# Optimization experiments

Hardware: AMD Instinct MI355X
Metric: run time of the kernel (lower is better)

Reference implementation:

```python
import jax, jax.numpy as jnp
import numpy as np

N = 50000   # nodes
E = 800000  # edges (avg degree 16)
DIMS = [(128, 128), (128, 128), (128, 64)]  # (in, out) per SAGEConv layer
EPS_BN = 1e-5
EPS_NORM = 1e-12


def _make_layer(key, din, dout):
    k1, k2 = jax.random.split(key)
    s = 1.0 / np.sqrt(din)
    return (
        jax.random.normal(k1, (dout, din), jnp.float32) * s,  # Wl: neighbor linear
        jnp.zeros((dout,), jnp.float32),                      # bl
        jax.random.normal(k2, (dout, din), jnp.float32) * s,  # Wr: root linear (no bias in PyG)
        jnp.ones((dout,), jnp.float32),                       # bn gamma
        jnp.zeros((dout,), jnp.float32),                      # bn beta
        jnp.zeros((dout,), jnp.float32),                      # bn running mean
        jnp.ones((dout,), jnp.float32),                       # bn running var
    )


def setup_inputs() -> dict:
    key = jax.random.key(0)
    kx, ke, k0, k1, k2 = jax.random.split(key, 5)
    inp = {
        "x": jax.random.normal(kx, (N, 128), jnp.float32),
        "edge_index": jax.random.randint(ke, (2, E), 0, N, dtype=jnp.int32),
    }
    for i, (k, (din, dout)) in enumerate(zip([k0, k1, k2], DIMS)):
        Wl, bl, Wr, g, b, rm, rv = _make_layer(k, din, dout)
        inp.update({f"Wl{i}": Wl, f"bl{i}": bl, f"Wr{i}": Wr,
                    f"g{i}": g, f"b{i}": b, f"rm{i}": rm, f"rv{i}": rv})
    return inp


def _sage_conv(x, src, dst, Wl, bl, Wr):
    # mean aggregation of incoming messages: gather src features, scatter-add at dst
    agg = jax.ops.segment_sum(x[src], dst, num_segments=N)          # [N, din]
    deg = jax.ops.segment_sum(jnp.ones((src.shape[0],), x.dtype), dst, num_segments=N)
    mean = agg / jnp.maximum(deg, 1.0)[:, None]
    return mean @ Wl.T + bl + x @ Wr.T


def _bn_eval(x, g, b, rm, rv):
    return g * (x - rm) * jax.lax.rsqrt(rv + EPS_BN) + b


def reference(x, edge_index,
              Wl0, bl0, Wr0, g0, b0, rm0, rv0,
              Wl1, bl1, Wr1, g1, b1, rm1, rv1,
              Wl2, bl2, Wr2, g2, b2, rm2, rv2):
    src, dst = edge_index[0], edge_index[1]
    layers = [
        (Wl0, bl0, Wr0, g0, b0, rm0, rv0),
        (Wl1, bl1, Wr1, g1, b1, rm1, rv1),
        (Wl2, bl2, Wr2, g2, b2, rm2, rv2),
    ]
    h = x
    for i, (Wl, bl, Wr, g, b, rm, rv) in enumerate(layers):
        h = _bn_eval(_sage_conv(h, src, dst, Wl, bl, Wr), g, b, rm, rv)
        if i < len(layers) - 1:
            h = jax.nn.relu(h)  # dropout is identity in eval mode
    # F.normalize(p=2, dim=1)
    return h / jnp.maximum(jnp.linalg.norm(h, axis=1, keepdims=True), EPS_NORM)
```

## Files before the change

### kernel.cpp

```cpp
#include <hip/hip_runtime.h>
#include <hip/hip_bf16.h>

#define CDIV(a,b) (((a)+(b)-1)/(b))
#define NBUCK_MAX 512
#define BUCK_CAP 3072
#define FUSE_CAP 1536
#define CAPL     4096
#define AGGF_CAP 2048

typedef __attribute__((ext_vector_type(8))) short short8;
typedef __attribute__((ext_vector_type(4))) float f32x4;
typedef __attribute__((ext_vector_type(2))) float f32x2;

static __device__ __forceinline__ unsigned short f2bf(float f){
  union { float f; unsigned u; } v; v.f = f;
  unsigned r = v.u + 0x7fffu + ((v.u >> 16) & 1u);
  return (unsigned short)(r >> 16);
}
static __device__ __forceinline__ unsigned pack2(float lo, float hi){
  return (unsigned)f2bf(lo) | ((unsigned)f2bf(hi) << 16);
}
static __device__ __forceinline__ float bf2f(unsigned short s){
  union { unsigned u; float f; } v; v.u = ((unsigned)s) << 16; return v.f;
}
static __device__ __forceinline__ unsigned pk_fp8x4(float a, float b, float c, float d){
  int v = __builtin_amdgcn_cvt_pk_fp8_f32(a, b, 0, false);
  v = __builtin_amdgcn_cvt_pk_fp8_f32(c, d, v, true);
  return (unsigned)v;
}

#define ACCP16(v) { b0 += __builtin_amdgcn_cvt_pk_f32_fp8((int)v.x, false); \
                    b1 += __builtin_amdgcn_cvt_pk_f32_fp8((int)v.x, true);  \
                    b2 += __builtin_amdgcn_cvt_pk_f32_fp8((int)v.y, false); \
                    b3 += __builtin_amdgcn_cvt_pk_f32_fp8((int)v.y, true);  \
                    b4 += __builtin_amdgcn_cvt_pk_f32_fp8((int)v.z, false); \
                    b5 += __builtin_amdgcn_cvt_pk_f32_fp8((int)v.z, true);  \
                    b6 += __builtin_amdgcn_cvt_pk_f32_fp8((int)v.w, false); \
                    b7 += __builtin_amdgcn_cvt_pk_f32_fp8((int)v.w, true); }


struct WtpArgs {
  const float *W0, *W1, *bl, *g, *b, *rm, *rv;
  unsigned short* Bpk; float *sc; float *sh;
  int kblk, dout, do_bn, nblk, perm;
};

static __device__ __forceinline__ void wtp_one(const WtpArgs& a, int idx){
  int NB16 = a.kblk*32*a.dout;
  if (idx < NB16){
    int j = idx & 7, lane = (idx >> 3) & 63, rest = idx >> 9;
    int NT = a.dout >> 4;
    int nt = rest % NT, kk = rest / NT;
    int nn = nt*16 + (lane & 15);
    int k  = kk*32 + ((lane >> 4) * 8) + j;
    float v;
    if (k < 128){
      int kc = a.perm ? (((k & 7) << 4) | (k >> 3)) : k;
      v = a.W0[nn*128 + kc];
    } else {
      v = a.W1[nn*128 + (k - 128)];
    }
    a.Bpk[idx] = f2bf(v);
  } else if (a.do_bn && idx < NB16 + a.dout){
    int jj = idx - NB16;
    float s = a.g[jj] * rsqrtf(a.rv[jj] + 1e-5f);
    a.sc[jj] = s;
    a.sh[jj] = (a.bl[jj] - a.rm[jj]) * s + a.b[jj];
  }
}


__global__ __launch_bounds__(256) void k_prep(const float* __restrict__ x, int n4, unsigned* __restrict__ xb,
                                              unsigned* __restrict__ xq,
                                              const int* __restrict__ esrc, const int* __restrict__ edst,
                                              int E, int* __restrict__ bcur, int* __restrict__ ovCnt,
                                              unsigned* __restrict__ ebuf, unsigned* __restrict__ ovBuf,
                                              int nbuck, int castBlocks, int binBlocks,
                                              WtpArgs a0, WtpArgs a1, WtpArgs a2, WtpArgs a3){
  __shared__ int scnt[NBUCK_MAX];
  __shared__ int sbase[NBUCK_MAX];
  int b = blockIdx.x, t = threadIdx.x;
  if (b < castBlocks){
    int i0 = b*1024 + t;
    #pragma unroll
    for (int j=0;j<4;j++){
      int i = i0 + j*256;
      if (i < n4){
        float4 v = ((const float4*)x)[i];
        uint2 o; o.x = pack2(v.x, v.y); o.y = pack2(v.z, v.w);
        ((uint2*)xb)[i] = o;
        xq[i] = pk_fp8x4(v.x, v.y, v.z, v.w);
      }
    }
    return;
  }
  b -= castBlocks;
  if (b < binBlocks){
    for (int i=t;i<nbuck;i+=256) scnt[i] = 0;
    __syncthreads();
    constexpr int EPT = 16;
    int e0 = b*256*EPT;
    int bb[EPT]; unsigned pk[EPT];
    #pragma unroll
    for (int i=0;i<EPT;i++){
      int e = e0 + i*256 + t;
      if (e < E){
        int d = edst[e];
        bb[i] = d >> 7;
        pk[i] = ((unsigned)(d & 127) << 16) | (unsigned)esrc[e];
        atomicAdd(&scnt[bb[i]], 1);
      } else bb[i] = -1;
    }
    __syncthreads();
    for (int i=t;i<nbuck;i+=256){
      int c = scnt[i];
      sbase[i] = (c > 0) ? atomicAdd(&bcur[i], c) : 0;
      scnt[i] = 0;
    }
    __syncthreads();
    #pragma unroll
    for (int i=0;i<EPT;i++){
      if (bb[i] >= 0){
        int p = atomicAdd(&scnt[bb[i]], 1);
        int gpos = sbase[bb[i]] + p;
        if (gpos < BUCK_CAP) ebuf[(size_t)bb[i]*BUCK_CAP + gpos] = pk[i];
        else { int oi = atomicAdd(ovCnt, 1); ovBuf[oi] = ((unsigned)bb[i] << 23) | pk[i]; }
      }
    }
    return;
  }
  b -= binBlocks;
  if (b < a0.nblk){ wtp_one(a0, b*256 + t); return; }
  b -= a0.nblk;
  if (b < a1.nblk){ wtp_one(a1, b*256 + t); return; }
  b -= a1.nblk;
  if (b < a2.nblk){ wtp_one(a2, b*256 + t); return; }
  b -= a2.nblk;
  wtp_one(a3, b*256 + t);
}


__global__ __launch_bounds__(256, 4) void k_bfuse(
    const unsigned* __restrict__ ebuf, const int* __restrict__ bcur,
    const int* __restrict__ ovCnt, const unsigned* __restrict__ ovBuf, int N,
    int* __restrict__ off, int* __restrict__ deg, int* __restrict__ csr,
    const uint4* __restrict__ xq4, const unsigned short* __restrict__ Ag,
    const unsigned short* __restrict__ Bpk, const float* __restrict__ sc, const float* __restrict__ sh,
    unsigned short* __restrict__ outh, unsigned* __restrict__ outq){
  __shared__ uint4 Ms4[64*17];
  __shared__ int scsr[FUSE_CAP];
  unsigned short* Ms = (unsigned short*)Ms4;
  int* sdeg = (int*)Ms4;
  int* sabs = sdeg + 128;
  int* cur  = sabs + 129;
  int wb = blockIdx.x;
  int b = wb >> 1, hi = wb & 1;
  int t = threadIdx.x;
  if (t < 128){ sdeg[t] = 0; cur[t] = 0; }
  __syncthreads();
  size_t bBase = (size_t)b*BUCK_CAP;
  int cntMain = min(bcur[b], BUCK_CAP);
  int ov = *ovCnt;
  for (int e = t; e < cntMain; e += 256)
    atomicAdd(&sdeg[ebuf[bBase + e] >> 16], 1);
  for (int i = t; i < ov; i += 256){
    unsigned v = ovBuf[i];
    if ((int)(v >> 23) == b) atomicAdd(&sdeg[(v >> 16) & 127u], 1);
  }
  __syncthreads();
  for (int d=1; d<128; d<<=1){
    int u = (t < 128 && t >= d) ? sdeg[t-d] : 0;
    __syncthreads();
    if (t < 128) sdeg[t] += u;
    __syncthreads();
  }
  if (t == 0) sabs[0] = 0;
  if (t < 128) sabs[t+1] = sdeg[t];
  __syncthreads();
  int base64 = sabs[hi*64];
  int myTot  = sabs[hi*64 + 64] - base64;
  int n0 = (b << 7) + hi*64;
  int cnt = (N > n0) ? min(64, N - n0) : 0;
  if (t < cnt){
    off[n0 + t] = (int)bBase + sabs[hi*64 + t];
    deg[n0 + t] = sabs[hi*64 + t + 1] - sabs[hi*64 + t];
  }
  int lane = t & 63, w = t >> 6, sl = lane & 7;
  int gs0[2], gs1[2];
  #pragma unroll
  for (int it=0; it<2; it++){
    int rk = w*16 + it*8 + (lane >> 3);
    gs0[it] = sabs[hi*64 + rk] - base64;
    gs1[it] = sabs[hi*64 + rk + 1] - base64;
  }
  bool fits = myTot <= FUSE_CAP;
  for (int e = t; e < cntMain; e += 256){
    unsigned pr = ebuf[bBase + e];
    int ln = (int)(pr >> 16);
    if ((ln >> 6) == hi){
      int p = atomicAdd(&cur[ln], 1);
      int gpos = sabs[ln] + p;
      int sv = (int)(pr & 0xffffu);
      if (fits) scsr[gpos - base64] = sv;
      else      csr[bBase + gpos] = sv;
    }
  }
  for (int i = t; i < ov; i += 256){
    unsigned v = ovBuf[i];
    if ((int)(v >> 23) == b){
      int ln = (int)((v >> 16) & 127u);
      if ((ln >> 6) == hi){
        int p = atomicAdd(&cur[ln], 1);
        int gpos = sabs[ln] + p;
        int sv = (int)(v & 0xffffu);
        if (fits) scsr[gpos - base64] = sv;
        else      csr[bBase + gpos] = sv;
      }
    }
  }
  __syncthreads();
  const int* gcsr = csr + bBase + base64;
  if (fits){
    for (int i = t; i < myTot; i += 256) csr[bBase + base64 + i] = scsr[i];
  } else {
    for (int i = t; i < FUSE_CAP; i += 256) scsr[i] = gcsr[i];
    __syncthreads();
  }

  #pragma unroll
  for (int it=0; it<2; it++){
    int rk = w*16 + it*8 + (lane >> 3);
    int s0 = gs0[it], s1 = gs1[it];
    f32x2 b0={0,0},b1={0,0},b2={0,0},b3={0,0},b4={0,0},b5={0,0},b6={0,0},b7={0,0};
    int e = s0;
    for (; e + 8 <= s1; e += 8){
      int i0,i1,i2,i3,i4,i5,i6,i7;
      if (e + 8 <= FUSE_CAP){
        i0 = scsr[e];   i1 = scsr[e+1]; i2 = scsr[e+2]; i3 = scsr[e+3];
        i4 = scsr[e+4]; i5 = scsr[e+5]; i6 = scsr[e+6]; i7 = scsr[e+7];
      } else {
        i0 = gcsr[e];   i1 = gcsr[e+1]; i2 = gcsr[e+2]; i3 = gcsr[e+3];
        i4 = gcsr[e+4]; i5 = gcsr[e+5]; i6 = gcsr[e+6]; i7 = gcsr[e+7];
      }
      uint4 v0 = xq4[(size_t)i0*8 + sl];
      uint4 v1 = xq4[(size_t)i1*8 + sl];
      uint4 v2 = xq4[(size_t)i2*8 + sl];
      uint4 v3 = xq4[(size_t)i3*8 + sl];
      uint4 v4 = xq4[(size_t)i4*8 + sl];
      uint4 v5 = xq4[(size_t)i5*8 + sl];
      uint4 v6 = xq4[(size_t)i6*8 + sl];
      uint4 v7 = xq4[(size_t)i7*8 + sl];
      ACCP16(v0); ACCP16(v1); ACCP16(v2); ACCP16(v3);
      ACCP16(v4); ACCP16(v5); ACCP16(v6); ACCP16(v7);
    }
    for (; e + 4 <= s1; e += 4){
      int i0,i1,i2,i3;
      if (e + 4 <= FUSE_CAP){
        i0 = scsr[e]; i1 = scsr[e+1]; i2 = scsr[e+2]; i3 = scsr[e+3];
      } else {
        i0 = gcsr[e]; i1 = gcsr[e+1]; i2 = gcsr[e+2]; i3 = gcsr[e+3];
      }
      uint4 v0 = xq4[(size_t)i0*8 + sl];
      uint4 v1 = xq4[(size_t)i1*8 + sl];
      uint4 v2 = xq4[(size_t)i2*8 + sl];
      uint4 v3 = xq4[(size_t)i3*8 + sl];
      ACCP16(v0); ACCP16(v1); ACCP16(v2); ACCP16(v3);
    }
    for (; e < s1; e++){
      int ii = (e < FUSE_CAP) ? scsr[e] : gcsr[e];
      uint4 v = xq4[(size_t)ii*8 + sl];
      ACCP16(v);
    }
    int d = s1 - s0;
    float inv = 1.0f / (float)(d > 0 ? d : 1);
    uint4 o0, o1;
    o0.x = pack2(b0.x*inv, b0.y*inv);  o0.y = pack2(b1.x*inv, b1.y*inv);
    o0.z = pack2(b2.x*inv, b2.y*inv);  o0.w = pack2(b3.x*inv, b3.y*inv);
    o1.x = pack2(b4.x*inv, b4.y*inv);  o1.y = pack2(b5.x*inv, b5.y*inv);
    o1.z = pack2(b6.x*inv, b6.y*inv);  o1.w = pack2(b7.x*inv, b7.y*inv);
    Ms4[rk*17 + sl*2]     = o0;
    Ms4[rk*17 + sl*2 + 1] = o1;
  }
  __syncthreads();

  int quad = lane >> 4, c = lane & 15;
  int woff = w*16;
  int r0 = n0 + woff + c;

  f32x4 acc[8];
  #pragma unroll
  for (int nt=0;nt<8;nt++) acc[nt] = (f32x4){0.f,0.f,0.f,0.f};

  #pragma unroll
  for (int kk=0; kk<8; kk++){
    int ka = (kk & 3)*32 + quad*8;
    short8 a0;
    if (kk < 4){
      a0 = *(const short8*)&Ms[(woff + c)*136 + ka];
    } else {
      a0 = (short8){0,0,0,0,0,0,0,0};
      if (r0 < N) a0 = *(const short8*)(Ag + (size_t)r0*128 + ka);
    }
    #pragma unroll
    for (int nt=0; nt<8; nt++){
      short8 bb2 = *(const short8*)(Bpk + (size_t)((kk*8 + nt)*64 + lane)*8);
      acc[nt] = __builtin_amdgcn_mfma_f32_16x16x32_bf16(a0, bb2, acc[nt], 0, 0, 0);
    }
  }

  float scv[8], shv[8];
  #pragma unroll
  for (int nt=0;nt<8;nt++){ scv[nt] = sc[nt*16 + c]; shv[nt] = sh[nt*16 + c]; }

  #pragma unroll
  for (int r=0;r<4;r++){
    int row = n0 + woff + quad*4 + r;
    if (row < N){
      float u[8];
      #pragma unroll
      for (int nt=0;nt<8;nt++){
        float uu = acc[nt][r]*scv[nt] + shv[nt];
        u[nt] = fmaxf(uu, 0.f);
        outh[(size_t)row*128 + nt*16 + c] = f2bf(u[nt]);
      }
      uint2 q;
      q.x = pk_fp8x4(u[0], u[1], u[2], u[3]);
      q.y = pk_fp8x4(u[4], u[5], u[6], u[7]);
      ((uint2*)outq)[(size_t)row*16 + c] = q;
    }
  }
}


__global__ __launch_bounds__(256, 4) void k_fuse1(
    const uint4* __restrict__ hq4, const int* __restrict__ off, const int* __restrict__ deg,
    const int* __restrict__ csr,
    const unsigned short* __restrict__ Ag, const unsigned short* __restrict__ Bpk,
    const float* __restrict__ sc, const float* __restrict__ sh,
    const unsigned short* __restrict__ BpkL,
    unsigned short* __restrict__ outh, unsigned* __restrict__ outyl, int n){
  __shared__ uint4 Ms4[64*17];
  __shared__ uint4 sBL4[1024];
  __shared__ int sw[2];
  unsigned short* Ms = (unsigned short*)Ms4;
  int* scsr = (int*)sBL4;
  int t = threadIdx.x;
  int n0 = blockIdx.x*64;
  if (t == 0){
    sw[0] = off[n0];
    int last = min(n0 + 63, n - 1);
    sw[1] = off[last] + deg[last];
  }
  __syncthreads();
  int e0b = sw[0];
  int span = sw[1] - e0b;
  for (int i = t; i < span && i < CAPL; i += 256) scsr[i] = csr[e0b + i];
  __syncthreads();

  int lane = t & 63, w = t >> 6;
  int sl = lane & 7;

  #pragma unroll
  for (int it=0; it<2; it++){
    int rk = w*16 + it*8 + (lane >> 3);
    int idx = n0 + rk;
    bool valid = idx < n;
    int s0 = valid ? off[idx] : 0;
    int s1 = valid ? (s0 + deg[idx]) : 0;
    f32x2 b0={0,0},b1={0,0},b2={0,0},b3={0,0},b4={0,0},b5={0,0},b6={0,0},b7={0,0};
    int e = s0;
    for (; e + 8 <= s1; e += 8){
      int le = e - e0b;
      int i0,i1,i2,i3,i4,i5,i6,i7;
      if (le + 8 <= CAPL){
        i0 = scsr[le];   i1 = scsr[le+1]; i2 = scsr[le+2]; i3 = scsr[le+3];
        i4 = scsr[le+4]; i5 = scsr[le+5]; i6 = scsr[le+6]; i7 = scsr[le+7];
      } else {
        i0 = csr[e];   i1 = csr[e+1]; i2 = csr[e+2]; i3 = csr[e+3];
        i4 = csr[e+4]; i5 = csr[e+5]; i6 = csr[e+6]; i7 = csr[e+7];
      }
      uint4 v0 = hq4[(size_t)i0*8 + sl];
      uint4 v1 = hq4[(size_t)i1*8 + sl];
      uint4 v2 = hq4[(size_t)i2*8 + sl];
      uint4 v3 = hq4[(size_t)i3*8 + sl];
      uint4 v4 = hq4[(size_t)i4*8 + sl];
      uint4 v5 = hq4[(size_t)i5*8 + sl];
      uint4 v6 = hq4[(size_t)i6*8 + sl];
      uint4 v7 = hq4[(size_t)i7*8 + sl];
      ACCP16(v0); ACCP16(v1); ACCP16(v2); ACCP16(v3);
      ACCP16(v4); ACCP16(v5); ACCP16(v6); ACCP16(v7);
    }
    for (; e + 4 <= s1; e += 4){
      int le = e - e0b;
      int i0,i1,i2,i3;
      if (le + 4 <= CAPL){
        i0 = scsr[le]; i1 = scsr[le+1]; i2 = scsr[le+2]; i3 = scsr[le+3];
      } else {
        i0 = csr[e]; i1 = csr[e+1]; i2 = csr[e+2]; i3 = csr[e+3];
      }
      uint4 v0 = hq4[(size_t)i0*8 + sl];
      uint4 v1 = hq4[(size_t)i1*8 + sl];
      uint4 v2 = hq4[(size_t)i2*8 + sl];
      uint4 v3 = hq4[(size_t)i3*8 + sl];
      ACCP16(v0); ACCP16(v1); ACCP16(v2); ACCP16(v3);
    }
    for (; e < s1; e++){
      int le = e - e0b;
      int ii = (le < CAPL) ? scsr[le] : csr[e];
      uint4 v = hq4[(size_t)ii*8 + sl];
      ACCP16(v);
    }
    int d = s1 - s0;
    float inv = 1.0f / (float)(d > 0 ? d : 1);
    uint4 o0, o1;
    o0.x = pack2(b0.x*inv, b0.y*inv);  o0.y = pack2(b1.x*inv, b1.y*inv);
    o0.z = pack2(b2.x*inv, b2.y*inv);  o0.w = pack2(b3.x*inv, b3.y*inv);
    o1.x = pack2(b4.x*inv, b4.y*inv);  o1.y = pack2(b5.x*inv, b5.y*inv);
    o1.z = pack2(b6.x*inv, b6.y*inv);  o1.w = pack2(b7.x*inv, b7.y*inv);
    Ms4[rk*17 + sl*2]     = o0;
    Ms4[rk*17 + sl*2 + 1] = o1;
  }
  __syncthreads();

  int quad = lane >> 4, c = lane & 15;
  int woff = w*16;
  int r0 = n0 + woff + c;

  f32x4 acc[8];
  #pragma unroll
  for (int nt=0;nt<8;nt++) acc[nt] = (f32x4){0.f,0.f,0.f,0.f};

  #pragma unroll
  for (int kk=0; kk<8; kk++){
    int ka = (kk & 3)*32 + quad*8;
    short8 a0;
    if (kk < 4){
      a0 = *(const short8*)&Ms[(woff + c)*136 + ka];
    } else {
      a0 = (short8){0,0,0,0,0,0,0,0};
      if (r0 < n) a0 = *(const short8*)(Ag + (size_t)r0*128 + ka);
    }
    #pragma unroll
    for (int nt=0; nt<8; nt++){
      short8 bb2 = *(const short8*)(Bpk + (size_t)((kk*8 + nt)*64 + lane)*8);
      acc[nt] = __builtin_amdgcn_mfma_f32_16x16x32_bf16(a0, bb2, acc[nt], 0, 0, 0);
    }
  }

  float scv[8], shv[8];
  #pragma unroll
  for (int nt=0;nt<8;nt++){ scv[nt] = sc[nt*16 + c]; shv[nt] = sh[nt*16 + c]; }

  __syncthreads();

  #pragma unroll
  for (int r=0;r<4;r++){
    int lrow = woff + quad*4 + r;
    int row = n0 + lrow;
    if (row < n){
      float u[8];
      #pragma unroll
      for (int nt=0;nt<8;nt++){
        float uu = acc[nt][r]*scv[nt] + shv[nt];
        u[nt] = fmaxf(uu, 0.f);
        outh[(size_t)row*128 + nt*16 + c] = f2bf(u[nt]);
      }
      #pragma unroll
      for (int nt=0;nt<8;nt++) Ms[lrow*136 + nt*16 + c] = f2bf(u[nt]);
    } else {
      #pragma unroll
      for (int nt=0;nt<8;nt++) Ms[lrow*136 + nt*16 + c] = 0;
    }
  }

  {
    const uint4* sL = (const uint4*)BpkL;
    #pragma unroll
    for (int i=0;i<4;i++) sBL4[i*256 + t] = sL[i*256 + t];
  }
  __syncthreads();
  unsigned short* BsL = (unsigned short*)sBL4;
  f32x4 acc2[4];
  #pragma unroll
  for (int nt=0;nt<4;nt++) acc2[nt] = (f32x4){0.f,0.f,0.f,0.f};
  int r0l = woff + c;
  #pragma unroll
  for (int kk=0; kk<4; kk++){
    int ka = kk*32 + quad*8;
    short8 a0 = *(const short8*)&Ms[r0l*136 + ka];
    #pragma unroll
    for (int nt=0; nt<4; nt++){
      short8 bb2 = *(const short8*)&BsL[(size_t)((kk*4 + nt)*64 + lane)*8];
      acc2[nt] = __builtin_amdgcn_mfma_f32_16x16x32_bf16(a0, bb2, acc2[nt], 0, 0, 0);
    }
  }
  #pragma unroll
  for (int r=0;r<4;r++){
    int row = n0 + woff + quad*4 + r;
    if (row < n){
      unsigned q = pk_fp8x4(acc2[0][r], acc2[1][r], acc2[2][r], acc2[3][r]);
      outyl[(size_t)row*16 + c] = q;
    }
  }
}


__global__ __launch_bounds__(256, 4) void k_aggf(
    const uint4* __restrict__ ylq4, const int* __restrict__ off, const int* __restrict__ deg,
    const int* __restrict__ csr,
    const unsigned short* __restrict__ A0, const unsigned short* __restrict__ BpkR,
    const float* __restrict__ sc, const float* __restrict__ sh,
    float* __restrict__ outf, int n){
  __shared__ unsigned short Ms[64*64];
  __shared__ unsigned short Bs[128*64];
  __shared__ int scsr[AGGF_CAP];
  __shared__ int sw[2];
  int t = threadIdx.x;
  int n0 = blockIdx.x*64;
  if (t == 0){
    sw[0] = off[n0];
    int last = min(n0 + 63, n - 1);
    sw[1] = off[last] + deg[last];
  }
  {
    const uint4* s = (const uint4*)BpkR;
    uint4* d = (uint4*)Bs;
    #pragma unroll
    for (int i=0;i<4;i++) d[i*256 + t] = s[i*256 + t];
  }
  __syncthreads();
  int e0b = sw[0];
  int span = sw[1] - e0b;
  for (int i = t; i < span && i < AGGF_CAP; i += 256) scsr[i] = csr[e0b + i];
  __syncthreads();

  int lane = t & 63, w = t >> 6;
  int sl4 = lane & 3;

  {
    int rk = w*16 + (lane >> 2);
    int idx = n0 + rk;
    bool valid = idx < n;
    int s0 = valid ? off[idx] : 0;
    int s1 = valid ? (s0 + deg[idx]) : 0;
    f32x2 b0={0,0},b1={0,0},b2={0,0},b3={0,0},b4={0,0},b5={0,0},b6={0,0},b7={0,0};
    int e = s0;
    for (; e + 8 <= s1; e += 8){
      int le = e - e0b;
      int i0,i1,i2,i3,i4,i5,i6,i7;
      if (le + 8 <= AGGF_CAP){
        i0 = scsr[le];   i1 = scsr[le+1]; i2 = scsr[le+2]; i3 = scsr[le+3];
        i4 = scsr[le+4]; i5 = scsr[le+5]; i6 = scsr[le+6]; i7 = scsr[le+7];
      } else {
        i0 = csr[e];   i1 = csr[e+1]; i2 = csr[e+2]; i3 = csr[e+3];
        i4 = csr[e+4]; i5 = csr[e+5]; i6 = csr[e+6]; i7 = csr[e+7];
      }
      uint4 v0 = ylq4[(size_t)i0*4 + sl4];
      uint4 v1 = ylq4[(size_t)i1*4 + sl4];
      uint4 v2 = ylq4[(size_t)i2*4 + sl4];
      uint4 v3 = ylq4[(size_t)i3*4 + sl4];
      uint4 v4 = ylq4[(size_t)i4*4 + sl4];
      uint4 v5 = ylq4[(size_t)i5*4 + sl4];
      uint4 v6 = ylq4[(size_t)i6*4 + sl4];
      uint4 v7 = ylq4[(size_t)i7*4 + sl4];
      ACCP16(v0); ACCP16(v1); ACCP16(v2); ACCP16(v3);
      ACCP16(v4); ACCP16(v5); ACCP16(v6); ACCP16(v7);
    }
    for (; e + 4 <= s1; e += 4){
      int le = e - e0b;
      int i0,i1,i2,i3;
      if (le + 4 <= AGGF_CAP){
        i0 = scsr[le]; i1 = scsr[le+1]; i2 = scsr[le+2]; i3 = scsr[le+3];
      } else {
        i0 = csr[e]; i1 = csr[e+1]; i2 = csr[e+2]; i3 = csr[e+3];
      }
      uint4 v0 = ylq4[(size_t)i0*4 + sl4];
      uint4 v1 = ylq4[(size_t)i1*4 + sl4];
      uint4 v2 = ylq4[(size_t)i2*4 + sl4];
      uint4 v3 = ylq4[(size_t)i3*4 + sl4];
      ACCP16(v0); ACCP16(v1); ACCP16(v2); ACCP16(v3);
    }
    for (; e < s1; e++){
      int le = e - e0b;
      int ii = (le < AGGF_CAP) ? scsr[le] : csr[e];
      uint4 v = ylq4[(size_t)ii*4 + sl4];
      ACCP16(v);
    }
    int d = s1 - s0;
    float inv = 1.0f / (float)(d > 0 ? d : 1);
    uint4 o0, o1;
    o0.x = pack2(b0.x*inv, b0.y*inv);  o0.y = pack2(b1.x*inv, b1.y*inv);
    o0.z = pack2(b2.x*inv, b2.y*inv);  o0.w = pack2(b3.x*inv, b3.y*inv);
    o1.x = pack2(b4.x*inv, b4.y*inv);  o1.y = pack2(b5.x*inv, b5.y*inv);
    o1.z = pack2(b6.x*inv, b6.y*inv);  o1.w = pack2(b7.x*inv, b7.y*inv);
    ((uint4*)Ms)[rk*8 + sl4*2]     = o0;
    ((uint4*)Ms)[rk*8 + sl4*2 + 1] = o1;
  }
  __syncthreads();

  int quad = lane >> 4, c = lane & 15;
  int woff = w*16;
  int r0 = n0 + woff + c;
  f32x4 acc[4];
  #pragma unroll
  for (int nt=0;nt<4;nt++) acc[nt] = (f32x4){0.f,0.f,0.f,0.f};
  #pragma unroll
  for (int kk=0; kk<4; kk++){
    int ka = kk*32 + quad*8;
    short8 a0 = {0,0,0,0,0,0,0,0};
    if (r0 < n) a0 = *(const short8*)(A0 + (size_t)r0*128 + ka);
    #pragma unroll
    for (int nt=0; nt<4; nt++){
      short8 bb2 = *(const short8*)&Bs[(size_t)((kk*4 + nt)*64 + lane)*8];
      acc[nt] = __builtin_amdgcn_mfma_f32_16x16x32_bf16(a0, bb2, acc[nt], 0, 0, 0);
    }
  }

  float scv[4], shv[4];
  #pragma unroll
  for (int nt=0;nt<4;nt++){ scv[nt] = sc[nt*16 + c]; shv[nt] = sh[nt*16 + c]; }

  #pragma unroll
  for (int r=0;r<4;r++){
    int lr = woff + quad*4 + r;
    int row = n0 + lr;
    float v[4];
    float ss2 = 0.f;
    if (row < n){
      #pragma unroll
      for (int nt=0;nt<4;nt++){
        float u = acc[nt][r] + bf2f(Ms[lr*64 + c*4 + nt]);
        u = u*scv[nt] + shv[nt];
        v[nt] = u;
        ss2 += u*u;
      }
    } else {
      #pragma unroll
      for (int nt=0;nt<4;nt++) v[nt] = 0.f;
    }
    ss2 += __shfl_xor(ss2, 1, 64);
    ss2 += __shfl_xor(ss2, 2, 64);
    ss2 += __shfl_xor(ss2, 4, 64);
    ss2 += __shfl_xor(ss2, 8, 64);
    float rn = 1.0f / fmaxf(sqrtf(ss2), 1e-12f);
    if (row < n){
      #pragma unroll
      for (int nt=0;nt<4;nt++) outf[(size_t)row*64 + nt*16 + c] = v[nt]*rn;
    }
  }
}


extern "C" void kernel_launch(void* const* d_in, const int* in_sizes, int n_in,
                              void* d_out, int out_size, void* d_ws, size_t ws_size,
                              hipStream_t stream){
  const float* x = (const float*)d_in[0];
  const int* ei  = (const int*)d_in[1];
  int N = in_sizes[0] / 128;
  int E = in_sizes[1] / 2;
  const int* esrc = ei;
  const int* edst = ei + E;
  int nbuck = CDIV(N, 128);
  int nb2 = 2*nbuck;

  const float *Wl[3], *bl[3], *Wr[3], *g[3], *bb[3], *rm[3], *rv[3];
  int dout[3];
  for (int i=0;i<3;i++){
    int base = 2 + 7*i;
    Wl[i]=(const float*)d_in[base];   bl[i]=(const float*)d_in[base+1];
    Wr[i]=(const float*)d_in[base+2]; g[i] =(const float*)d_in[base+3];
    bb[i]=(const float*)d_in[base+4]; rm[i]=(const float*)d_in[base+5];
    rv[i]=(const float*)d_in[base+6];
    dout[i] = in_sizes[base] / 128;
  }

  char* p = (char*)d_ws;
  size_t o = 0;
  auto alloc = [&](size_t bytes)->void*{ void* r = p + o; o += (bytes + 255) & ~(size_t)255; return r; };
  int* bz    = (int*)alloc((size_t)(nbuck + 1)*4);
  int* bcur  = bz;
  int* ovCnt = bz + nbuck;
  int* off   = (int*)alloc((size_t)N*4);
  int* deg   = (int*)alloc((size_t)N*4);
  int* csr   = (int*)alloc((size_t)nbuck*BUCK_CAP*4);
  unsigned* ebuf  = (unsigned*)alloc((size_t)nbuck*BUCK_CAP*4);
  unsigned* ovBuf = (unsigned*)alloc((size_t)E*4);
  unsigned* xb   = (unsigned*)alloc((size_t)N*64*4);
  unsigned* xq   = (unsigned*)alloc((size_t)N*128);
  unsigned* h_a  = (unsigned*)alloc((size_t)N*64*4);
  unsigned* haq  = (unsigned*)alloc((size_t)N*128);
  unsigned* h_b  = (unsigned*)alloc((size_t)N*64*4);
  unsigned* ylb  = (unsigned*)alloc((size_t)N*64);
  unsigned short* Bpk01[2];
  float* sc[3]; float* sh[3];
  for (int i=0;i<2;i++) Bpk01[i] = (unsigned short*)alloc((size_t)256*dout[i]*2);
  unsigned short* BpkL = (unsigned short*)alloc((size_t)128*dout[2]*2);
  unsigned short* BpkR = (unsigned short*)alloc((size_t)128*dout[2]*2);
  for (int i=0;i<3;i++){
    sc[i] = (float*)alloc((size_t)dout[i]*4);
    sh[i] = (float*)alloc((size_t)dout[i]*4);
  }

  hipMemsetAsync(bz, 0, (size_t)(nbuck + 1)*4, stream);

  WtpArgs wa[4];
  wa[0] = { Wl[0], Wr[0], bl[0], g[0], bb[0], rm[0], rv[0], Bpk01[0], sc[0], sh[0], 8, dout[0], 1, CDIV(256*dout[0]+dout[0],256), 0 };
  wa[1] = { Wl[1], Wr[1], bl[1], g[1], bb[1], rm[1], rv[1], Bpk01[1], sc[1], sh[1], 8, dout[1], 1, CDIV(256*dout[1]+dout[1],256), 1 };
  wa[2] = { Wl[2], nullptr, nullptr, nullptr, nullptr, nullptr, nullptr, BpkL, nullptr, nullptr, 4, dout[2], 0, CDIV(128*dout[2],256), 0 };
  wa[3] = { Wr[2], nullptr, bl[2], g[2], bb[2], rm[2], rv[2], BpkR, sc[2], sh[2], 4, dout[2], 1, CDIV(128*dout[2]+dout[2],256), 0 };

  int castBlocks = CDIV(N*32, 256*4);
  int binBlocks  = CDIV(E, 256*16);
  int prepBlocks = castBlocks + binBlocks + wa[0].nblk + wa[1].nblk + wa[2].nblk + wa[3].nblk;
  k_prep<<<prepBlocks,256,0,stream>>>(x, N*32, xb, xq, esrc, edst, E, bcur, ovCnt, ebuf, ovBuf,
                                      nbuck, castBlocks, binBlocks,
                                      wa[0], wa[1], wa[2], wa[3]);

  k_bfuse<<<nb2,256,0,stream>>>(ebuf, bcur, ovCnt, ovBuf, N, off, deg, csr,
                                (const uint4*)xq, (const unsigned short*)xb,
                                Bpk01[0], sc[0], sh[0],
                                (unsigned short*)h_a, haq);
  k_fuse1<<<nb2,256,0,stream>>>((const uint4*)haq, off, deg, csr,
                                (const unsigned short*)h_a, Bpk01[1], sc[1], sh[1], BpkL,
                                (unsigned short*)h_b, ylb, N);
  k_aggf<<<nb2,256,0,stream>>>((const uint4*)ylb, off, deg, csr,
                               (const unsigned short*)h_b, BpkR, sc[2], sh[2],
                               (float*)d_out, N);
}
```

Measured before the change: 209.6 us.

## Replace bucketed CSR build with fixed-capacity per-node 16-bit adjacency slots

```diff
diff --git a/kernel.cpp b/kernel.cpp
--- a/kernel.cpp
+++ b/kernel.cpp
@@ -2,11 +2,7 @@
 #include <hip/hip_bf16.h>
 
 #define CDIV(a,b) (((a)+(b)-1)/(b))
-#define NBUCK_MAX 512
-#define BUCK_CAP 3072
-#define FUSE_CAP 1536
-#define CAPL     4096
-#define AGGF_CAP 2048
+#define NODE_CAP 64
 
 typedef __attribute__((ext_vector_type(8))) short short8;
 typedef __attribute__((ext_vector_type(4))) float f32x4;
@@ -37,6 +33,11 @@
                     b5 += __builtin_amdgcn_cvt_pk_f32_fp8((int)v.z, true);  \
                     b6 += __builtin_amdgcn_cvt_pk_f32_fp8((int)v.w, false); \
                     b7 += __builtin_amdgcn_cvt_pk_f32_fp8((int)v.w, true); }
+
+#define IDX8(iv) int i0 = (int)(iv.x & 0xffffu), i1 = (int)(iv.x >> 16), \
+                     i2 = (int)(iv.y & 0xffffu), i3 = (int)(iv.y >> 16), \
+                     i4 = (int)(iv.z & 0xffffu), i5 = (int)(iv.z >> 16), \
+                     i6 = (int)(iv.w & 0xffffu), i7 = (int)(iv.w >> 16)
 
 
 struct WtpArgs {
@@ -73,12 +74,10 @@
 __global__ __launch_bounds__(256) void k_prep(const float* __restrict__ x, int n4, unsigned* __restrict__ xb,
                                               unsigned* __restrict__ xq,
                                               const int* __restrict__ esrc, const int* __restrict__ edst,
-                                              int E, int* __restrict__ bcur, int* __restrict__ ovCnt,
-                                              unsigned* __restrict__ ebuf, unsigned* __restrict__ ovBuf,
-                                              int nbuck, int castBlocks, int binBlocks,
+                                              int E, int* __restrict__ deg, int* __restrict__ ovCnt,
+                                              unsigned short* __restrict__ csr16, unsigned* __restrict__ ovBuf,
+                                              int castBlocks, int binBlocks,
                                               WtpArgs a0, WtpArgs a1, WtpArgs a2, WtpArgs a3){
-  __shared__ int scnt[NBUCK_MAX];
-  __shared__ int sbase[NBUCK_MAX];
   int b = blockIdx.x, t = threadIdx.x;
   if (b < castBlocks){
     int i0 = b*1024 + t;
@@ -96,35 +95,17 @@
   }
   b -= castBlocks;
   if (b < binBlocks){
-    for (int i=t;i<nbuck;i+=256) scnt[i] = 0;
-    __syncthreads();
     constexpr int EPT = 16;
     int e0 = b*256*EPT;
-    int bb[EPT]; unsigned pk[EPT];
     #pragma unroll
     for (int i=0;i<EPT;i++){
       int e = e0 + i*256 + t;
       if (e < E){
         int d = edst[e];
-        bb[i] = d >> 7;
-        pk[i] = ((unsigned)(d & 127) << 16) | (unsigned)esrc[e];
-        atomicAdd(&scnt[bb[i]], 1);
-      } else bb[i] = -1;
-    }
-    __syncthreads();
-    for (int i=t;i<nbuck;i+=256){
-      int c = scnt[i];
-      sbase[i] = (c > 0) ? atomicAdd(&bcur[i], c) : 0;
-      scnt[i] = 0;
-    }
-    __syncthreads();
-    #pragma unroll
-    for (int i=0;i<EPT;i++){
-      if (bb[i] >= 0){
-        int p = atomicAdd(&scnt[bb[i]], 1);
-        int gpos = sbase[bb[i]] + p;
-        if (gpos < BUCK_CAP) ebuf[(size_t)bb[i]*BUCK_CAP + gpos] = pk[i];
-        else { int oi = atomicAdd(ovCnt, 1); ovBuf[oi] = ((unsigned)bb[i] << 23) | pk[i]; }
+        int s = esrc[e];
+        int p = atomicAdd(&deg[d], 1);
+        if (p < NODE_CAP) csr16[(size_t)d*NODE_CAP + p] = (unsigned short)s;
+        else { int oi = atomicAdd(ovCnt, 1); ovBuf[oi] = ((unsigned)d << 16) | (unsigned)s; }
       }
     }
     return;
@@ -140,108 +121,39 @@
 }
 
 
-__global__ __launch_bounds__(256, 4) void k_bfuse(
-    const unsigned* __restrict__ ebuf, const int* __restrict__ bcur,
+__global__ __launch_bounds__(256, 4) void k_fuse0(
+    const unsigned short* __restrict__ csr16, const int* __restrict__ deg,
     const int* __restrict__ ovCnt, const unsigned* __restrict__ ovBuf, int N,
-    int* __restrict__ off, int* __restrict__ deg, int* __restrict__ csr,
     const uint4* __restrict__ xq4, const unsigned short* __restrict__ Ag,
     const unsigned short* __restrict__ Bpk, const float* __restrict__ sc, const float* __restrict__ sh,
     unsigned short* __restrict__ outh, unsigned* __restrict__ outq){
   __shared__ uint4 Ms4[64*17];
-  __shared__ int scsr[FUSE_CAP];
+  __shared__ uint4 sc4[512];
   unsigned short* Ms = (unsigned short*)Ms4;
-  int* sdeg = (int*)Ms4;
-  int* sabs = sdeg + 128;
-  int* cur  = sabs + 129;
-  int wb = blockIdx.x;
-  int b = wb >> 1, hi = wb & 1;
+  unsigned short* scsr = (unsigned short*)sc4;
   int t = threadIdx.x;
-  if (t < 128){ sdeg[t] = 0; cur[t] = 0; }
-  __syncthreads();
-  size_t bBase = (size_t)b*BUCK_CAP;
-  int cntMain = min(bcur[b], BUCK_CAP);
+  int n0 = blockIdx.x*64;
+  {
+    const uint4* s = (const uint4*)(csr16 + (size_t)n0*NODE_CAP);
+    sc4[t] = s[t];
+    sc4[256 + t] = s[256 + t];
+  }
+  __syncthreads();
+
+  int lane = t & 63, w = t >> 6, sl = lane & 7;
   int ov = *ovCnt;
-  for (int e = t; e < cntMain; e += 256)
-    atomicAdd(&sdeg[ebuf[bBase + e] >> 16], 1);
-  for (int i = t; i < ov; i += 256){
-    unsigned v = ovBuf[i];
-    if ((int)(v >> 23) == b) atomicAdd(&sdeg[(v >> 16) & 127u], 1);
-  }
-  __syncthreads();
-  for (int d=1; d<128; d<<=1){
-    int u = (t < 128 && t >= d) ? sdeg[t-d] : 0;
-    __syncthreads();
-    if (t < 128) sdeg[t] += u;
-    __syncthreads();
-  }
-  if (t == 0) sabs[0] = 0;
-  if (t < 128) sabs[t+1] = sdeg[t];
-  __syncthreads();
-  int base64 = sabs[hi*64];
-  int myTot  = sabs[hi*64 + 64] - base64;
-  int n0 = (b << 7) + hi*64;
-  int cnt = (N > n0) ? min(64, N - n0) : 0;
-  if (t < cnt){
-    off[n0 + t] = (int)bBase + sabs[hi*64 + t];
-    deg[n0 + t] = sabs[hi*64 + t + 1] - sabs[hi*64 + t];
-  }
-  int lane = t & 63, w = t >> 6, sl = lane & 7;
-  int gs0[2], gs1[2];
+
   #pragma unroll
   for (int it=0; it<2; it++){
     int rk = w*16 + it*8 + (lane >> 3);
-    gs0[it] = sabs[hi*64 + rk] - base64;
-    gs1[it] = sabs[hi*64 + rk + 1] - base64;
-  }
-  bool fits = myTot <= FUSE_CAP;
-  for (int e = t; e < cntMain; e += 256){
-    unsigned pr = ebuf[bBase + e];
-    int ln = (int)(pr >> 16);
-    if ((ln >> 6) == hi){
-      int p = atomicAdd(&cur[ln], 1);
-      int gpos = sabs[ln] + p;
-      int sv = (int)(pr & 0xffffu);
-      if (fits) scsr[gpos - base64] = sv;
-      else      csr[bBase + gpos] = sv;
-    }
-  }
-  for (int i = t; i < ov; i += 256){
-    unsigned v = ovBuf[i];
-    if ((int)(v >> 23) == b){
-      int ln = (int)((v >> 16) & 127u);
-      if ((ln >> 6) == hi){
-        int p = atomicAdd(&cur[ln], 1);
-        int gpos = sabs[ln] + p;
-        int sv = (int)(v & 0xffffu);
-        if (fits) scsr[gpos - base64] = sv;
-        else      csr[bBase + gpos] = sv;
-      }
-    }
-  }
-  __syncthreads();
-  const int* gcsr = csr + bBase + base64;
-  if (fits){
-    for (int i = t; i < myTot; i += 256) csr[bBase + base64 + i] = scsr[i];
-  } else {
-    for (int i = t; i < FUSE_CAP; i += 256) scsr[i] = gcsr[i];
-    __syncthreads();
-  }
-
-  #pragma unroll
-  for (int it=0; it<2; it++){
-    int rk = w*16 + it*8 + (lane >> 3);
-    int s0 = gs0[it], s1 = gs1[it];
+    int node = n0 + rk;
+    int d = (node < N) ? deg[node] : 0;
+    int dmin = min(d, NODE_CAP);
     f32x2 b0={0,0},b1={0,0},b2={0,0},b3={0,0},b4={0,0},b5={0,0},b6={0,0},b7={0,0};
-    int e = s0;
-    for (; e + 8 <= s1; e += 8){
-      int i0,i1,i2,i3,i4,i5,i6,i7;
-      if (e + 8 <= FUSE_CAP){
-        i0 = scsr[e];   i1 = scsr[e+1]; i2 = scsr[e+2]; i3 = scsr[e+3];
-        i4 = scsr[e+4]; i5 = scsr[e+5]; i6 = scsr[e+6]; i7 = scsr[e+7];
-      } else {
-        i0 = gcsr[e];   i1 = gcsr[e+1]; i2 = gcsr[e+2]; i3 = gcsr[e+3];
-        i4 = gcsr[e+4]; i5 = gcsr[e+5]; i6 = gcsr[e+6]; i7 = gcsr[e+7];
-      }
+    int e = 0;
+    for (; e + 8 <= dmin; e += 8){
+      uint4 iv = *(const uint4*)&scsr[rk*NODE_CAP + e];
+      IDX8(iv);
       uint4 v0 = xq4[(size_t)i0*8 + sl];
       uint4 v1 = xq4[(size_t)i1*8 + sl];
       uint4 v2 = xq4[(size_t)i2*8 + sl];
@@ -253,25 +165,20 @@
       ACCP16(v0); ACCP16(v1); ACCP16(v2); ACCP16(v3);
       ACCP16(v4); ACCP16(v5); ACCP16(v6); ACCP16(v7);
     }
-    for (; e + 4 <= s1; e += 4){
-      int i0,i1,i2,i3;
-      if (e + 4 <= FUSE_CAP){
-        i0 = scsr[e]; i1 = scsr[e+1]; i2 = scsr[e+2]; i3 = scsr[e+3];
-      } else {
-        i0 = gcsr[e]; i1 = gcsr[e+1]; i2 = gcsr[e+2]; i3 = gcsr[e+3];
-      }
-      uint4 v0 = xq4[(size_t)i0*8 + sl];
-      uint4 v1 = xq4[(size_t)i1*8 + sl];
-      uint4 v2 = xq4[(size_t)i2*8 + sl];
-      uint4 v3 = xq4[(size_t)i3*8 + sl];
-      ACCP16(v0); ACCP16(v1); ACCP16(v2); ACCP16(v3);
-    }
-    for (; e < s1; e++){
-      int ii = (e < FUSE_CAP) ? scsr[e] : gcsr[e];
+    for (; e < dmin; e++){
+      int ii = (int)scsr[rk*NODE_CAP + e];
       uint4 v = xq4[(size_t)ii*8 + sl];
       ACCP16(v);
     }
-    int d = s1 - s0;
+    if (ov > 0 && d > NODE_CAP){
+      for (int i=0;i<ov;i++){
+        unsigned vv = ovBuf[i];
+        if ((int)(vv >> 16) == node){
+          uint4 v = xq4[(size_t)(vv & 0xffffu)*8 + sl];
+          ACCP16(v);
+        }
+      }
+    }
     float inv = 1.0f / (float)(d > 0 ? d : 1);
     uint4 o0, o1;
     o0.x = pack2(b0.x*inv, b0.y*inv);  o0.y = pack2(b1.x*inv, b1.y*inv);
@@ -333,52 +240,39 @@
 
 
 __global__ __launch_bounds__(256, 4) void k_fuse1(
-    const uint4* __restrict__ hq4, const int* __restrict__ off, const int* __restrict__ deg,
-    const int* __restrict__ csr,
+    const uint4* __restrict__ hq4, const unsigned short* __restrict__ csr16, const int* __restrict__ deg,
+    const int* __restrict__ ovCnt, const unsigned* __restrict__ ovBuf,
     const unsigned short* __restrict__ Ag, const unsigned short* __restrict__ Bpk,
     const float* __restrict__ sc, const float* __restrict__ sh,
     const unsigned short* __restrict__ BpkL,
     unsigned short* __restrict__ outh, unsigned* __restrict__ outyl, int n){
   __shared__ uint4 Ms4[64*17];
   __shared__ uint4 sBL4[1024];
-  __shared__ int sw[2];
   unsigned short* Ms = (unsigned short*)Ms4;
-  int* scsr = (int*)sBL4;
+  unsigned short* scsr = (unsigned short*)sBL4;
   int t = threadIdx.x;
   int n0 = blockIdx.x*64;
-  if (t == 0){
-    sw[0] = off[n0];
-    int last = min(n0 + 63, n - 1);
-    sw[1] = off[last] + deg[last];
-  }
-  __syncthreads();
-  int e0b = sw[0];
-  int span = sw[1] - e0b;
-  for (int i = t; i < span && i < CAPL; i += 256) scsr[i] = csr[e0b + i];
-  __syncthreads();
-
-  int lane = t & 63, w = t >> 6;
-  int sl = lane & 7;
+  {
+    const uint4* s = (const uint4*)(csr16 + (size_t)n0*NODE_CAP);
+    sBL4[t] = s[t];
+    sBL4[256 + t] = s[256 + t];
+  }
+  __syncthreads();
+
+  int lane = t & 63, w = t >> 6, sl = lane & 7;
+  int ov = *ovCnt;
 
   #pragma unroll
   for (int it=0; it<2; it++){
     int rk = w*16 + it*8 + (lane >> 3);
-    int idx = n0 + rk;
-    bool valid = idx < n;
-    int s0 = valid ? off[idx] : 0;
-    int s1 = valid ? (s0 + deg[idx]) : 0;
+    int node = n0 + rk;
+    int d = (node < n) ? deg[node] : 0;
+    int dmin = min(d, NODE_CAP);
     f32x2 b0={0,0},b1={0,0},b2={0,0},b3={0,0},b4={0,0},b5={0,0},b6={0,0},b7={0,0};
-    int e = s0;
-    for (; e + 8 <= s1; e += 8){
-      int le = e - e0b;
-      int i0,i1,i2,i3,i4,i5,i6,i7;
-      if (le + 8 <= CAPL){
-        i0 = scsr[le];   i1 = scsr[le+1]; i2 = scsr[le+2]; i3 = scsr[le+3];
-        i4 = scsr[le+4]; i5 = scsr[le+5]; i6 = scsr[le+6]; i7 = scsr[le+7];
-      } else {
-        i0 = csr[e];   i1 = csr[e+1]; i2 = csr[e+2]; i3 = csr[e+3];
-        i4 = csr[e+4]; i5 = csr[e+5]; i6 = csr[e+6]; i7 = csr[e+7];
-      }
+    int e = 0;
+    for (; e + 8 <= dmin; e += 8){
+      uint4 iv = *(const uint4*)&scsr[rk*NODE_CAP + e];
+      IDX8(iv);
       uint4 v0 = hq4[(size_t)i0*8 + sl];
       uint4 v1 = hq4[(size_t)i1*8 + sl];
       uint4 v2 = hq4[(size_t)i2*8 + sl];
@@ -390,27 +284,20 @@
       ACCP16(v0); ACCP16(v1); ACCP16(v2); ACCP16(v3);
       ACCP16(v4); ACCP16(v5); ACCP16(v6); ACCP16(v7);
     }
-    for (; e + 4 <= s1; e += 4){
-      int le = e - e0b;
-      int i0,i1,i2,i3;
-      if (le + 4 <= CAPL){
-        i0 = scsr[le]; i1 = scsr[le+1]; i2 = scsr[le+2]; i3 = scsr[le+3];
-      } else {
-        i0 = csr[e]; i1 = csr[e+1]; i2 = csr[e+2]; i3 = csr[e+3];
-      }
-      uint4 v0 = hq4[(size_t)i0*8 + sl];
-      uint4 v1 = hq4[(size_t)i1*8 + sl];
-      uint4 v2 = hq4[(size_t)i2*8 + sl];
-      uint4 v3 = hq4[(size_t)i3*8 + sl];
-      ACCP16(v0); ACCP16(v1); ACCP16(v2); ACCP16(v3);
-    }
-    for (; e < s1; e++){
-      int le = e - e0b;
-      int ii = (le < CAPL) ? scsr[le] : csr[e];
+    for (; e < dmin; e++){
+      int ii = (int)scsr[rk*NODE_CAP + e];
       uint4 v = hq4[(size_t)ii*8 + sl];
       ACCP16(v);
     }
-    int d = s1 - s0;
+    if (ov > 0 && d > NODE_CAP){
+      for (int i=0;i<ov;i++){
+        unsigned vv = ovBuf[i];
+        if ((int)(vv >> 16) == node){
+          uint4 v = hq4[(size_t)(vv & 0xffffu)*8 + sl];
+          ACCP16(v);
+        }
+      }
+    }
     float inv = 1.0f / (float)(d > 0 ? d : 1);
     uint4 o0, o1;
     o0.x = pack2(b0.x*inv, b0.y*inv);  o0.y = pack2(b1.x*inv, b1.y*inv);
@@ -506,55 +393,44 @@
 
 
 __global__ __launch_bounds__(256, 4) void k_aggf(
-    const uint4* __restrict__ ylq4, const int* __restrict__ off, const int* __restrict__ deg,
-    const int* __restrict__ csr,
+    const uint4* __restrict__ ylq4, const unsigned short* __restrict__ csr16, const int* __restrict__ deg,
+    const int* __restrict__ ovCnt, const unsigned* __restrict__ ovBuf,
     const unsigned short* __restrict__ A0, const unsigned short* __restrict__ BpkR,
     const float* __restrict__ sc, const float* __restrict__ sh,
     float* __restrict__ outf, int n){
   __shared__ unsigned short Ms[64*64];
   __shared__ unsigned short Bs[128*64];
-  __shared__ int scsr[AGGF_CAP];
-  __shared__ int sw[2];
+  __shared__ uint4 sc4[512];
+  unsigned short* scsr = (unsigned short*)sc4;
   int t = threadIdx.x;
   int n0 = blockIdx.x*64;
-  if (t == 0){
-    sw[0] = off[n0];
-    int last = min(n0 + 63, n - 1);
-    sw[1] = off[last] + deg[last];
+  {
+    const uint4* s = (const uint4*)(csr16 + (size_t)n0*NODE_CAP);
+    sc4[t] = s[t];
+    sc4[256 + t] = s[256 + t];
   }
   {
     const uint4* s = (const uint4*)BpkR;
-    uint4* d = (uint4*)Bs;
-    #pragma unroll
-    for (int i=0;i<4;i++) d[i*256 + t] = s[i*256 + t];
-  }
-  __syncthreads();
-  int e0b = sw[0];
-  int span = sw[1] - e0b;
-  for (int i = t; i < span && i < AGGF_CAP; i += 256) scsr[i] = csr[e0b + i];
+    uint4* dd = (uint4*)Bs;
+    #pragma unroll
+    for (int i=0;i<4;i++) dd[i*256 + t] = s[i*256 + t];
+  }
   __syncthreads();
 
   int lane = t & 63, w = t >> 6;
   int sl4 = lane & 3;
+  int ov = *ovCnt;
 
   {
     int rk = w*16 + (lane >> 2);
-    int idx = n0 + rk;
-    bool valid = idx < n;
-    int s0 = valid ? off[idx] : 0;
-    int s1 = valid ? (s0 + deg[idx]) : 0;
+    int node = n0 + rk;
+    int d = (node < n) ? deg[node] : 0;
+    int dmin = min(d, NODE_CAP);
     f32x2 b0={0,0},b1={0,0},b2={0,0},b3={0,0},b4={0,0},b5={0,0},b6={0,0},b7={0,0};
-    int e = s0;
-    for (; e + 8 <= s1; e += 8){
-      int le = e - e0b;
-      int i0,i1,i2,i3,i4,i5,i6,i7;
-      if (le + 8 <= AGGF_CAP){
-        i0 = scsr[le];   i1 = scsr[le+1]; i2 = scsr[le+2]; i3 = scsr[le+3];
-        i4 = scsr[le+4]; i5 = scsr[le+5]; i6 = scsr[le+6]; i7 = scsr[le+7];
-      } else {
-        i0 = csr[e];   i1 = csr[e+1]; i2 = csr[e+2]; i3 = csr[e+3];
-        i4 = csr[e+4]; i5 = csr[e+5]; i6 = csr[e+6]; i7 = csr[e+7];
-      }
+    int e = 0;
+    for (; e + 8 <= dmin; e += 8){
+      uint4 iv = *(const uint4*)&scsr[rk*NODE_CAP + e];
+      IDX8(iv);
       uint4 v0 = ylq4[(size_t)i0*4 + sl4];
       uint4 v1 = ylq4[(size_t)i1*4 + sl4];
       uint4 v2 = ylq4[(size_t)i2*4 + sl4];
@@ -566,27 +442,20 @@
       ACCP16(v0); ACCP16(v1); ACCP16(v2); ACCP16(v3);
       ACCP16(v4); ACCP16(v5); ACCP16(v6); ACCP16(v7);
     }
-    for (; e + 4 <= s1; e += 4){
-      int le = e - e0b;
-      int i0,i1,i2,i3;
-      if (le + 4 <= AGGF_CAP){
-        i0 = scsr[le]; i1 = scsr[le+1]; i2 = scsr[le+2]; i3 = scsr[le+3];
-      } else {
-        i0 = csr[e]; i1 = csr[e+1]; i2 = csr[e+2]; i3 = csr[e+3];
-      }
-      uint4 v0 = ylq4[(size_t)i0*4 + sl4];
-      uint4 v1 = ylq4[(size_t)i1*4 + sl4];
-      uint4 v2 = ylq4[(size_t)i2*4 + sl4];
-      uint4 v3 = ylq4[(size_t)i3*4 + sl4];
-      ACCP16(v0); ACCP16(v1); ACCP16(v2); ACCP16(v3);
-    }
-    for (; e < s1; e++){
-      int le = e - e0b;
-      int ii = (le < AGGF_CAP) ? scsr[le] : csr[e];
+    for (; e < dmin; e++){
+      int ii = (int)scsr[rk*NODE_CAP + e];
       uint4 v = ylq4[(size_t)ii*4 + sl4];
       ACCP16(v);
     }
-    int d = s1 - s0;
+    if (ov > 0 && d > NODE_CAP){
+      for (int i=0;i<ov;i++){
+        unsigned vv = ovBuf[i];
+        if ((int)(vv >> 16) == node){
+          uint4 v = ylq4[(size_t)(vv & 0xffffu)*4 + sl4];
+          ACCP16(v);
+        }
+      }
+    }
     float inv = 1.0f / (float)(d > 0 ? d : 1);
     uint4 o0, o1;
     o0.x = pack2(b0.x*inv, b0.y*inv);  o0.y = pack2(b1.x*inv, b1.y*inv);
@@ -660,8 +529,8 @@
   int E = in_sizes[1] / 2;
   const int* esrc = ei;
   const int* edst = ei + E;
-  int nbuck = CDIV(N, 128);
-  int nb2 = 2*nbuck;
+  int nb2 = CDIV(N, 64);
+  int N2  = nb2 * 64;
 
   const float *Wl[3], *bl[3], *Wr[3], *g[3], *bb[3], *rm[3], *rv[3];
   int dout[3];
@@ -677,14 +546,11 @@
   char* p = (char*)d_ws;
   size_t o = 0;
   auto alloc = [&](size_t bytes)->void*{ void* r = p + o; o += (bytes + 255) & ~(size_t)255; return r; };
-  int* bz    = (int*)alloc((size_t)(nbuck + 1)*4);
-  int* bcur  = bz;
-  int* ovCnt = bz + nbuck;
-  int* off   = (int*)alloc((size_t)N*4);
-  int* deg   = (int*)alloc((size_t)N*4);
-  int* csr   = (int*)alloc((size_t)nbuck*BUCK_CAP*4);
-  unsigned* ebuf  = (unsigned*)alloc((size_t)nbuck*BUCK_CAP*4);
-  unsigned* ovBuf = (unsigned*)alloc((size_t)E*4);
+  int* bz    = (int*)alloc((size_t)(N2 + 1)*4);
+  int* deg   = bz;
+  int* ovCnt = bz + N2;
+  unsigned short* csr16 = (unsigned short*)alloc((size_t)N2*NODE_CAP*2);
+  unsigned* ovBuf = (unsigned*)alloc((size_t)4096*4);
   unsigned* xb   = (unsigned*)alloc((size_t)N*64*4);
   unsigned* xq   = (unsigned*)alloc((size_t)N*128);
   unsigned* h_a  = (unsigned*)alloc((size_t)N*64*4);
@@ -701,7 +567,7 @@
     sh[i] = (float*)alloc((size_t)dout[i]*4);
   }
 
-  hipMemsetAsync(bz, 0, (size_t)(nbuck + 1)*4, stream);
+  hipMemsetAsync(bz, 0, (size_t)(N2 + 1)*4, stream);
 
   WtpArgs wa[4];
   wa[0] = { Wl[0], Wr[0], bl[0], g[0], bb[0], rm[0], rv[0], Bpk01[0], sc[0], sh[0], 8, dout[0], 1, CDIV(256*dout[0]+dout[0],256), 0 };
@@ -712,18 +578,18 @@
   int castBlocks = CDIV(N*32, 256*4);
   int binBlocks  = CDIV(E, 256*16);
   int prepBlocks = castBlocks + binBlocks + wa[0].nblk + wa[1].nblk + wa[2].nblk + wa[3].nblk;
-  k_prep<<<prepBlocks,256,0,stream>>>(x, N*32, xb, xq, esrc, edst, E, bcur, ovCnt, ebuf, ovBuf,
-                                      nbuck, castBlocks, binBlocks,
+  k_prep<<<prepBlocks,256,0,stream>>>(x, N*32, xb, xq, esrc, edst, E, deg, ovCnt, csr16, ovBuf,
+                                      castBlocks, binBlocks,
                                       wa[0], wa[1], wa[2], wa[3]);
 
-  k_bfuse<<<nb2,256,0,stream>>>(ebuf, bcur, ovCnt, ovBuf, N, off, deg, csr,
+  k_fuse0<<<nb2,256,0,stream>>>(csr16, deg, ovCnt, ovBuf, N,
                                 (const uint4*)xq, (const unsigned short*)xb,
                                 Bpk01[0], sc[0], sh[0],
                                 (unsigned short*)h_a, haq);
-  k_fuse1<<<nb2,256,0,stream>>>((const uint4*)haq, off, deg, csr,
+  k_fuse1<<<nb2,256,0,stream>>>((const uint4*)haq, csr16, deg, ovCnt, ovBuf,
                                 (const unsigned short*)h_a, Bpk01[1], sc[1], sh[1], BpkL,
                                 (unsigned short*)h_b, ylb, N);
-  k_aggf<<<nb2,256,0,stream>>>((const uint4*)ylb, off, deg, csr,
+  k_aggf<<<nb2,256,0,stream>>>((const uint4*)ylb, csr16, deg, ovCnt, ovBuf,
                                (const unsigned short*)h_b, BpkR, sc[2], sh[2],
                                (float*)d_out, N);
 }
```

After: 228.8 us. 1.09x slower.
